# Performance work log

Measured on AMD Instinct MI355X. Metric: run time of the kernel, lower is better.

The kernel has to match this reference:

```python
import jax, jax.numpy as jnp
import numpy as np

D_MODEL = 1024
NUM_HEADS = 16
HEAD_DIM = D_MODEL // NUM_HEADS
B, S = 4, 2048


def setup_inputs() -> dict:
    key = jax.random.key(0)
    ks = jax.random.split(key, 11)
    sc = 1.0 / np.sqrt(D_MODEL)
    return {
        "query": jax.random.normal(ks[0], (B, S, D_MODEL), jnp.float32),
        "key": jax.random.normal(ks[1], (B, S, D_MODEL), jnp.float32),
        "value": jax.random.normal(ks[2], (B, S, D_MODEL), jnp.float32),
        "Wq": jax.random.normal(ks[3], (D_MODEL, D_MODEL), jnp.float32) * sc,
        "bq": jnp.zeros((D_MODEL,), jnp.float32),
        "Wk": jax.random.normal(ks[4], (D_MODEL, D_MODEL), jnp.float32) * sc,
        "bk": jnp.zeros((D_MODEL,), jnp.float32),
        "Wv": jax.random.normal(ks[5], (D_MODEL, D_MODEL), jnp.float32) * sc,
        "bv": jnp.zeros((D_MODEL,), jnp.float32),
        "Wo": jax.random.normal(ks[6], (D_MODEL, D_MODEL), jnp.float32) * sc,
        "bo": jnp.zeros((D_MODEL,), jnp.float32),
    }


def _split_heads(x):
    b, s, _ = x.shape
    return x.reshape(b, s, NUM_HEADS, HEAD_DIM).transpose(0, 2, 1, 3)  # [B,H,S,Dh]


def reference(query, key, value, Wq, bq, Wk, bk, Wv, bv, Wo, bo):
    q = _split_heads(query @ Wq + bq)
    k = _split_heads(key @ Wk + bk)
    v = _split_heads(value @ Wv + bv)
    scores = jnp.einsum("bhqd,bhkd->bhqk", q, k) / np.sqrt(HEAD_DIM)
    attn = jax.nn.softmax(scores, axis=-1)
    out = jnp.einsum("bhqk,bhkd->bhqd", attn, v)
    out = out.transpose(0, 2, 1, 3).reshape(query.shape[0], -1, D_MODEL)
    return out @ Wo + bo
```

## Files before the change

kernel.cpp:

```cpp
#include <hip/hip_runtime.h>

typedef unsigned short u16;
typedef unsigned int   u32;
typedef unsigned long long u64;
typedef __attribute__((ext_vector_type(8))) short bf16x8;
typedef __attribute__((ext_vector_type(4))) float f32x4;

#define S_  2048
#define DH  64
#define DM  1024
#define BS  8192
#define CS  0.18033688011112042f

static __device__ __forceinline__ float bf2f(u16 v){ return __uint_as_float(((u32)v)<<16); }
static __device__ __forceinline__ u16 f2bf(float f){
  u32 x = __float_as_uint(f);
  return (u16)((x + 0x7fffu + ((x>>16)&1u)) >> 16);
}
#if __has_builtin(__builtin_amdgcn_cvt_pk_bf16_f32)
static __device__ __forceinline__ u32 pk2(float x, float y){
  typedef __attribute__((ext_vector_type(2))) __bf16 bf2v;
  union { bf2v v; u32 u; } c; c.v = __builtin_amdgcn_cvt_pk_bf16_f32(x, y); return c.u;
}
#else
static __device__ __forceinline__ u32 pk2(float x, float y){
  return (u32)f2bf(x) | ((u32)f2bf(y) << 16);
}
#endif
#if __has_builtin(__builtin_amdgcn_exp2f)
#define EXP2F(x) __builtin_amdgcn_exp2f(x)
#else
#define EXP2F(x) exp2f(x)
#endif

static __device__ __forceinline__ void dma16(const u16* g, const u16* l){
  __builtin_amdgcn_global_load_lds(
      (const __attribute__((address_space(1))) u32*)(u64)(uintptr_t)g,
      (__attribute__((address_space(3))) u32*)(u32)(u64)(uintptr_t)l, 16, 0, 0);
}

static __device__ __forceinline__ bf16x8 lds_frag(const u16* p){
  union { bf16x8 f; uint2 u[2]; } w;
  w.u[0] = *(const uint2*)(p);
  w.u[1] = *(const uint2*)(p+4);
  return w.f;
}
static __device__ __forceinline__ bf16x8 frag16v(const u16* p){
  union { bf16x8 f; uint4 u; } w;
  w.u = *(const uint4*)p;
  return w.f;
}
static __device__ __forceinline__ void stage16_bf(const u16* __restrict__ g, u16* s){
  uint4 a = *(const uint4*)g;
  uint4 b = *(const uint4*)(g+8);
  *(uint2*)(s+0)  = make_uint2(a.x,a.y);
  *(uint2*)(s+4)  = make_uint2(a.z,a.w);
  *(uint2*)(s+8)  = make_uint2(b.x,b.y);
  *(uint2*)(s+12) = make_uint2(b.z,b.w);
}
static __device__ __forceinline__ void stage16_f32(const float* __restrict__ g, u16* s){
  float4 a0 = ((const float4*)g)[0];
  float4 a1 = ((const float4*)g)[1];
  float4 a2 = ((const float4*)g)[2];
  float4 a3 = ((const float4*)g)[3];
  *(uint2*)(s+0)  = make_uint2(pk2(a0.x,a0.y), pk2(a0.z,a0.w));
  *(uint2*)(s+4)  = make_uint2(pk2(a1.x,a1.y), pk2(a1.z,a1.w));
  *(uint2*)(s+8)  = make_uint2(pk2(a2.x,a2.y), pk2(a2.z,a2.w));
  *(uint2*)(s+12) = make_uint2(pk2(a3.x,a3.y), pk2(a3.z,a3.w));
}

union AFU { bf16x8 f; u32 u[4]; };

__global__ __launch_bounds__(256) void transpose4(const void* __restrict__ i0,
    const void* __restrict__ i1, const void* __restrict__ i2, const void* __restrict__ i3,
    u16* o0, u16* o1, u16* o2, u16* o3, const int f32f){
  __shared__ u16 tile[32][33];
  int z = blockIdx.z;
  const void* in = z==0?i0 : z==1?i1 : z==2?i2 : i3;
  u16* out = z==0?o0 : z==1?o1 : z==2?o2 : o3;
  bool f32 = f32f != 0;
  int tx = threadIdx.x, ty = threadIdx.y;
  int c  = blockIdx.x*32 + tx;
  int r0 = blockIdx.y*32;
  for (int i=ty;i<32;i+=8){
    long off = (long)(r0+i)*DM + c;
    tile[i][tx] = f32 ? f2bf(((const float*)in)[off]) : ((const u16*)in)[off];
  }
  __syncthreads();
  int rr = r0 + tx, c0 = blockIdx.x*32;
  for (int i=ty;i<32;i+=8) out[(long)(c0+i)*DM + rr] = tile[tx][i];
}

__global__ __launch_bounds__(256) void gemm_qkv(
    const void* __restrict__ A0, const void* __restrict__ A1, const void* __restrict__ A2,
    const u16* __restrict__ W0, const u16* __restrict__ W1, const u16* __restrict__ W2,
    const void* __restrict__ bv0, const void* __restrict__ bv1, const void* __restrict__ bv2,
    u16* C0, u16* C1, u16* C2, const int f32f){
  constexpr int AST = 36;
  __shared__ __align__(16) u16 As[128*AST];
  __shared__ __align__(16) u16 Bs[128*32];
  int z = blockIdx.z;
  const void* A  = z==0?A0 : z==1?A1 : A2;
  const u16* BT  = z==0?W0 : z==1?W1 : W2;
  const void* bias = z==0?bv0 : z==1?bv1 : bv2;
  u16* C = z==0?C0 : z==1?C1 : C2;
  const bool aF32 = (f32f != 0);
  int tid = threadIdx.x;
  int by = blockIdx.x, bx = blockIdx.y;
  int lane = tid & 63, w = tid >> 6;
  int t = lane & 15, q = lane >> 4;
  int wr = w >> 1, wc = w & 1;
  f32x4 acc[4][4];
  #pragma unroll
  for(int i=0;i<4;i++) for(int j=0;j<4;j++) for(int k=0;k<4;k++) acc[i][j][k]=0.f;

  const u16* gB = BT + ((long)(bx*128 + w*32 + (lane>>2))*DM + (lane&3)*8);
  const u16* lB = &Bs[(w*32)*32];
  long aoff = (long)(by*128 + (tid>>1))*DM + (tid&1)*16;
  const u16* ArdB = &As[(wr*64 + t)*AST + q*8];
  const u16* BrdB = &Bs[(wc*64 + t)*32  + q*8];

  for (int k0=0; k0<DM; k0+=32){
    dma16(gB + k0, lB);
    dma16(gB + 16*DM + k0, lB + 16*32);
    u16* AsW = &As[(tid>>1)*36 + (tid&1)*16];
    if (aF32) stage16_f32((const float*)A + aoff + k0, AsW);
    else      stage16_bf ((const u16*)A  + aoff + k0, AsW);
    __syncthreads();
    bf16x8 af[4], bfr[4];
    #pragma unroll
    for (int rt=0;rt<4;rt++) af[rt]  = lds_frag(ArdB + rt*16*AST);
    #pragma unroll
    for (int ct=0;ct<4;ct++) bfr[ct] = lds_frag(BrdB + ct*16*32);
    #pragma unroll
    for (int rt=0;rt<4;rt++)
      #pragma unroll
      for (int ct=0;ct<4;ct++)
        acc[rt][ct] = __builtin_amdgcn_mfma_f32_16x16x32_bf16(af[rt], bfr[ct], acc[rt][ct], 0,0,0);
    __syncthreads();
  }
  float scale = (z==0) ? CS : 1.0f;
  #pragma unroll
  for (int ct=0;ct<4;ct++){
    int col = bx*128 + wc*64 + ct*16 + t;
    float bvv = aF32 ? ((const float*)bias)[col] : bf2f(((const u16*)bias)[col]);
    #pragma unroll
    for (int rt=0;rt<4;rt++){
      int row0 = by*128 + wr*64 + rt*16 + q*4;
      if (z == 2){
        int bb = row0 >> 11, s = row0 & 2047;
        long vbase = (long)bb*2097152 + (long)col*2048
                   + (s & ~63) + ((rt>>1)<<5) + (q<<3) + ((rt&1)<<2);
        u32 lo = pk2(acc[rt][ct][0]+bvv, acc[rt][ct][1]+bvv);
        u32 hi = pk2(acc[rt][ct][2]+bvv, acc[rt][ct][3]+bvv);
        *(uint2*)(C + vbase) = make_uint2(lo,hi);
      } else {
        #pragma unroll
        for (int r=0;r<4;r++)
          C[(long)(row0+r)*DM + col] = f2bf((acc[rt][ct][r] + bvv)*scale);
      }
    }
  }
}

__global__ __launch_bounds__(256) void gemm_o(const u16* __restrict__ A,
    const u16* __restrict__ BT, const void* __restrict__ bias, void* __restrict__ C,
    const int f32f){
  __shared__ __align__(16) u16 As[128*32];
  __shared__ __align__(16) u16 Bs[128*32];
  const int f = f32f;
  int tid = threadIdx.x;
  int by = blockIdx.x, bx = blockIdx.y;
  int lane = tid & 63, w = tid >> 6;
  int t = lane & 15, q = lane >> 4;
  int wr = w >> 1, wc = w & 1;
  f32x4 acc[4][4];
  #pragma unroll
  for(int i=0;i<4;i++) for(int j=0;j<4;j++) for(int k=0;k<4;k++) acc[i][j][k]=0.f;

  const u16* gA = A  + ((long)(by*128 + w*32 + (lane>>2))*DM + (lane&3)*8);
  const u16* gB = BT + ((long)(bx*128 + w*32 + (lane>>2))*DM + (lane&3)*8);
  const u16* lA = &As[(w*32)*32];
  const u16* lB = &Bs[(w*32)*32];
  const u16* ArdB = &As[(wr*64 + t)*32 + q*8];
  const u16* BrdB = &Bs[(wc*64 + t)*32 + q*8];

  for (int k0=0; k0<DM; k0+=32){
    dma16(gA + k0, lA);
    dma16(gA + 16*DM + k0, lA + 16*32);
    dma16(gB + k0, lB);
    dma16(gB + 16*DM + k0, lB + 16*32);
    __syncthreads();
    bf16x8 af[4], bfr[4];
    #pragma unroll
    for (int rt=0;rt<4;rt++) af[rt]  = lds_frag(ArdB + rt*16*32);
    #pragma unroll
    for (int ct=0;ct<4;ct++) bfr[ct] = lds_frag(BrdB + ct*16*32);
    #pragma unroll
    for (int rt=0;rt<4;rt++)
      #pragma unroll
      for (int ct=0;ct<4;ct++)
        acc[rt][ct] = __builtin_amdgcn_mfma_f32_16x16x32_bf16(af[rt], bfr[ct], acc[rt][ct], 0,0,0);
    __syncthreads();
  }
  #pragma unroll
  for (int ct=0;ct<4;ct++){
    int col = bx*128 + wc*64 + ct*16 + t;
    float bvv = f ? ((const float*)bias)[col] : bf2f(((const u16*)bias)[col]);
    #pragma unroll
    for (int rt=0;rt<4;rt++){
      int row0 = by*128 + wr*64 + rt*16 + q*4;
      #pragma unroll
      for (int r=0;r<4;r++){
        long idx = (long)(row0+r)*DM + col;
        float v = acc[rt][ct][r] + bvv;
        if (f) ((float*)C)[idx] = v;
        else   ((u16*)C)[idx]  = f2bf(v);
      }
    }
  }
}

static __device__ __forceinline__ void qk16(const u16* Kc, int t, int q, int xorv,
    const bf16x8 (&qf)[2][2], f32x4 (&sacc)[2][4]){
  #pragma unroll
  for (int i=0;i<2;i++)
    #pragma unroll
    for (int j=0;j<4;j++)
      #pragma unroll
      for (int k=0;k<4;k++) sacc[i][j][k]=0.f;
  #pragma unroll
  for (int ks=0; ks<2; ks++){
    int off = ((ks*64 + q*16) ^ xorv) >> 1;
    bf16x8 k0 = frag16v(Kc + (t     )*64 + off);
    bf16x8 k1 = frag16v(Kc + (16 + t)*64 + off);
    bf16x8 k2 = frag16v(Kc + (32 + t)*64 + off);
    bf16x8 k3 = frag16v(Kc + (48 + t)*64 + off);
    __builtin_amdgcn_s_setprio(1);
    #pragma unroll
    for (int rt=0; rt<2; rt++){
      sacc[rt][0] = __builtin_amdgcn_mfma_f32_16x16x32_bf16(k0, qf[rt][ks], sacc[rt][0],0,0,0);
      sacc[rt][1] = __builtin_amdgcn_mfma_f32_16x16x32_bf16(k1, qf[rt][ks], sacc[rt][1],0,0,0);
      sacc[rt][2] = __builtin_amdgcn_mfma_f32_16x16x32_bf16(k2, qf[rt][ks], sacc[rt][2],0,0,0);
      sacc[rt][3] = __builtin_amdgcn_mfma_f32_16x16x32_bf16(k3, qf[rt][ks], sacc[rt][3],0,0,0);
    }
    __builtin_amdgcn_s_setprio(0);
  }
}

static __device__ __forceinline__ void sm16(const f32x4 (&sacc)[2][4], AFU (&af)[2][2]){
  #pragma unroll
  for (int rt=0; rt<2; rt++){
    float ev[4][4];
    #pragma unroll
    for (int c=0; c<4; c++)
      #pragma unroll
      for (int r=0; r<4; r++) ev[c][r] = EXP2F(sacc[rt][c][r]);
    #pragma unroll
    for (int ks=0; ks<2; ks++){
      af[rt][ks].u[0] = pk2(ev[2*ks  ][0], ev[2*ks  ][1]);
      af[rt][ks].u[1] = pk2(ev[2*ks  ][2], ev[2*ks  ][3]);
      af[rt][ks].u[2] = pk2(ev[2*ks+1][0], ev[2*ks+1][1]);
      af[rt][ks].u[3] = pk2(ev[2*ks+1][2], ev[2*ks+1][3]);
    }
  }
}

static __device__ __forceinline__ void pv16(const u16* Vc, int t, int q, int xorv,
    const AFU (&af)[2][2], bf16x8 vonef, f32x4 (&o)[2][4], f32x4 (&o4)[2]){
  #pragma unroll
  for (int ks=0; ks<2; ks++){
    int off = ((ks*64 + q*16) ^ xorv) >> 1;
    bf16x8 v0 = frag16v(Vc + (t     )*64 + off);
    bf16x8 v1 = frag16v(Vc + (16 + t)*64 + off);
    bf16x8 v2 = frag16v(Vc + (32 + t)*64 + off);
    bf16x8 v3 = frag16v(Vc + (48 + t)*64 + off);
    __builtin_amdgcn_s_setprio(1);
    #pragma unroll
    for (int rt=0; rt<2; rt++){
      o[rt][0] = __builtin_amdgcn_mfma_f32_16x16x32_bf16(af[rt][ks].f, v0, o[rt][0],0,0,0);
      o[rt][1] = __builtin_amdgcn_mfma_f32_16x16x32_bf16(af[rt][ks].f, v1, o[rt][1],0,0,0);
      o[rt][2] = __builtin_amdgcn_mfma_f32_16x16x32_bf16(af[rt][ks].f, v2, o[rt][2],0,0,0);
      o[rt][3] = __builtin_amdgcn_mfma_f32_16x16x32_bf16(af[rt][ks].f, v3, o[rt][3],0,0,0);
      o4[rt]   = __builtin_amdgcn_mfma_f32_16x16x32_bf16(af[rt][ks].f, vonef, o4[rt],0,0,0);
    }
    __builtin_amdgcn_s_setprio(0);
  }
}

__global__ __launch_bounds__(256,4) void attn6(const u16* __restrict__ Q,
    const u16* __restrict__ Kb, const u16* __restrict__ Vt, u16* __restrict__ O){
  __shared__ __align__(16) u16 SM_[20480];
  const int VB = 12288;
  int tid = threadIdx.x;
  int bid = blockIdx.x;
  int qt = bid >> 6;
  int s6 = bid & 63;
  int bh = (s6 & 7)*8 + (s6 >> 3);
  int b = bh >> 4, h = bh & 15;
  int lane = tid & 63, w = tid >> 6;
  int t = lane & 15, q = lane >> 4;

  const u16* Qbase = Q + ((long)(b*S_ + qt*128 + w*32 + t)*DM + h*DH + q*8);
  bf16x8 qf[2][2];
  qf[0][0] = frag16v(Qbase);
  qf[0][1] = frag16v(Qbase + 32);
  qf[1][0] = frag16v(Qbase + 16*DM);
  qf[1][1] = frag16v(Qbase + 16*DM + 32);

  int r0 = tid >> 3;
  int cb = ((tid & 7) * 16) ^ ((r0 & 7) << 4);
  const char* gK = (const char*)Kb + (((long)(b*S_ + r0)*DM + h*DH) << 1) + cb;
  const char* gV = (const char*)Vt + ((((long)bh << 17) + ((long)r0 << 11)) << 1) + cb;
  const long gK1 = ((long)32*DM) << 1;
  const long gV1 = ((long)32*S_) << 1;
  const long KT  = ((long)64*DM) << 1;
  const int ld0 = w*512, ld1 = 2048 + w*512;

  f32x4 o[2][4];
  #pragma unroll
  for (int i=0;i<2;i++)
    #pragma unroll
    for (int j=0;j<4;j++)
      #pragma unroll
      for (int k=0;k<4;k++) o[i][j][k]=0.f;
  f32x4 o4[2];
  #pragma unroll
  for (int i=0;i<2;i++)
    #pragma unroll
    for (int k=0;k<4;k++) o4[i][k]=0.f;

  union { bf16x8 f; u32 u[4]; } vone;
  { u32 ovv = (t==0) ? 0x3F803F80u : 0u;
    vone.u[0]=ovv; vone.u[1]=ovv; vone.u[2]=ovv; vone.u[3]=ovv; }

  const int xorv = (t & 7) << 4;

  dma16((const u16*)(gK),            &SM_[ld0]);
  dma16((const u16*)(gK + gK1),      &SM_[ld1]);
  dma16((const u16*)(gV),            &SM_[VB + ld0]);
  dma16((const u16*)(gV + gV1),      &SM_[VB + ld1]);
  dma16((const u16*)(gK + KT),       &SM_[4096 + ld0]);
  dma16((const u16*)(gK + KT + gK1), &SM_[4096 + ld1]);
  asm volatile("s_waitcnt vmcnt(4)" ::: "memory");
  __builtin_amdgcn_s_barrier();

  f32x4 sacc[2][4];
  AFU af[2][2];
  qk16(&SM_[0], t, q, xorv, qf, sacc);
  sm16(sacc, af);
  dma16((const u16*)(gK + 2*KT),       &SM_[8192 + ld0]);
  dma16((const u16*)(gK + 2*KT + gK1), &SM_[8192 + ld1]);
  dma16((const u16*)(gV + (1L<<7)),        &SM_[VB + 4096 + ld0]);
  dma16((const u16*)(gV + (1L<<7) + gV1),  &SM_[VB + 4096 + ld1]);

  int kcur = 4096, knx = 8192, kfree = 0;
  for (int kt = 1; kt < 32; kt++){
    asm volatile("s_waitcnt vmcnt(4)" ::: "memory");
    __builtin_amdgcn_s_barrier();
    if (kt <= 30){
      int nk = (kt+2 < 32) ? (kt+2) : 31;
      const char* g = gK + (long)nk*KT;
      dma16((const u16*)(g),       &SM_[kfree + ld0]);
      dma16((const u16*)(g + gK1), &SM_[kfree + ld1]);
    }
    qk16(&SM_[kcur], t, q, xorv, qf, sacc);
    pv16(&SM_[VB + (((kt-1)&1)<<12)], t, q, xorv, af, vone.f, o, o4);
    sm16(sacc, af);
    __builtin_amdgcn_s_barrier();
    if (kt <= 30){
      const char* g = gV + ((long)(kt+1) << 7);
      dma16((const u16*)(g),       &SM_[VB + (((kt+1)&1)<<12) + ld0]);
      dma16((const u16*)(g + gV1), &SM_[VB + (((kt+1)&1)<<12) + ld1]);
    }
    int tmp = kcur; kcur = knx; knx = kfree; kfree = tmp;
  }
  asm volatile("s_waitcnt vmcnt(0)" ::: "memory");
  __builtin_amdgcn_s_barrier();
  pv16(&SM_[VB + 4096], t, q, xorv, af, vone.f, o, o4);

  #pragma unroll
  for (int rt=0; rt<2; rt++){
    #pragma unroll
    for (int r=0; r<4; r++){
      float l = __shfl(o4[rt][r], lane & 48);
      float inv = 1.f / l;
      int row = qt*128 + w*32 + rt*16 + q*4 + r;
      #pragma unroll
      for (int ct=0; ct<4; ct++)
        O[(long)(b*S_ + row)*DM + h*DH + ct*16 + t] = f2bf(o[rt][ct][r] * inv);
    }
  }
}

extern "C" void kernel_launch(void* const* d_in, const int* in_sizes, int n_in,
                              void* d_out, int out_size, void* d_ws, size_t ws_size,
                              hipStream_t stream){
  (void)n_in; (void)out_size; (void)ws_size;
  const void* xq = d_in[0];
  const void* xk = d_in[1];
  const void* xv = d_in[2];
  const void* Wq = d_in[3];
  const void* bq = d_in[4];
  const void* Wk = d_in[5];
  const void* bk = d_in[6];
  const void* Wv = d_in[7];
  const void* bv = d_in[8];
  const void* Wo = d_in[9];
  const void* bo = d_in[10];

  const long NT = (long)BS*DM;
  int f32f = 1;
  if (in_sizes && in_sizes[0] == (int)(NT*2)) f32f = 0;

  u16* base = (u16*)((char*)d_ws + 256);
  u16* Qb  = base;
  u16* Kbf = base + NT;
  u16* Vt  = base + 2*NT;
  u16* WqT = base + 3*NT;
  u16* WkT = WqT + (long)DM*DM;
  u16* WvT = WkT + (long)DM*DM;
  u16* WoT = WvT + (long)DM*DM;

  dim3 gb(256,1,1);
  transpose4<<<dim3(32,32,4), dim3(32,8,1), 0, stream>>>(Wq, Wk, Wv, Wo,
      WqT, WkT, WvT, WoT, f32f);

  gemm_qkv<<<dim3(64,8,3), gb, 0, stream>>>(xq, xk, xv,
      WqT, WkT, WvT, bq, bk, bv, Qb, Kbf, Vt, f32f);

  attn6<<<dim3(1024,1,1), gb, 0, stream>>>(Qb, Kbf, Vt, Qb );

  gemm_o<<<dim3(64,8,1), gb, 0, stream>>>(Qb, WoT, bo, d_out, f32f);
}
```

Before: 403.7 us.

## Pre-convert activations to bf16 and double-buffer DMA in projection GEMMs

The weight-transpose kernel becomes a prep kernel that also converts the fp32 query/key/value activations to bf16 in workspace. When the workspace is large enough, the QKV GEMM can then load A through the same async DMA path as B. Both QKV and output GEMMs now double-buffer LDS and prefetch the next K-slice while computing the current one, using waitcnt and raw barriers. This adds an extra full pass over the activations and needs more workspace, in exchange for overlapping global loads with MFMA work.

```diff
diff --git a/kernel.cpp b/kernel.cpp
--- a/kernel.cpp
+++ b/kernel.cpp
@@ -71,40 +71,63 @@
 
 union AFU { bf16x8 f; u32 u[4]; };
 
-__global__ __launch_bounds__(256) void transpose4(const void* __restrict__ i0,
-    const void* __restrict__ i1, const void* __restrict__ i2, const void* __restrict__ i3,
-    u16* o0, u16* o1, u16* o2, u16* o3, const int f32f){
+__global__ __launch_bounds__(256) void prep(
+    const void* __restrict__ w0, const void* __restrict__ w1,
+    const void* __restrict__ w2, const void* __restrict__ w3,
+    u16* t0, u16* t1, u16* t2, u16* t3,
+    const void* __restrict__ a0, const void* __restrict__ a1,
+    const void* __restrict__ a2,
+    u16* c0, u16* c1, u16* c2, const int f32f){
   __shared__ u16 tile[32][33];
   int z = blockIdx.z;
-  const void* in = z==0?i0 : z==1?i1 : z==2?i2 : i3;
-  u16* out = z==0?o0 : z==1?o1 : z==2?o2 : o3;
+  int tid = threadIdx.x;
   bool f32 = f32f != 0;
-  int tx = threadIdx.x, ty = threadIdx.y;
-  int c  = blockIdx.x*32 + tx;
-  int r0 = blockIdx.y*32;
-  for (int i=ty;i<32;i+=8){
-    long off = (long)(r0+i)*DM + c;
-    tile[i][tx] = f32 ? f2bf(((const float*)in)[off]) : ((const u16*)in)[off];
-  }
-  __syncthreads();
-  int rr = r0 + tx, c0 = blockIdx.x*32;
-  for (int i=ty;i<32;i+=8) out[(long)(c0+i)*DM + rr] = tile[tx][i];
-}
-
+  if (z < 4){
+    const void* in = z==0?w0 : z==1?w1 : z==2?w2 : w3;
+    u16* out = z==0?t0 : z==1?t1 : z==2?t2 : t3;
+    int tx = tid & 31, ty = tid >> 5;
+    int c  = blockIdx.x*32 + tx;
+    int r0 = blockIdx.y*32;
+    for (int i=ty;i<32;i+=8){
+      long off = (long)(r0+i)*DM + c;
+      tile[i][tx] = f32 ? f2bf(((const float*)in)[off]) : ((const u16*)in)[off];
+    }
+    __syncthreads();
+    int rr = r0 + tx, cb = blockIdx.x*32;
+    for (int i=ty;i<32;i+=8) out[(long)(cb+i)*DM + rr] = tile[tx][i];
+  } else {
+    if (!f32) return;
+    const void* in = z==4?a0 : z==5?a1 : a2;
+    u16* out = z==4?c0 : z==5?c1 : c2;
+    long lb = (long)blockIdx.y*32 + blockIdx.x;
+    long base = (lb*256 + tid)*8;
+    #pragma unroll
+    for (int it=0; it<4; it++){
+      long i = base + (long)it*2097152;
+      const float4* p = (const float4*)((const float*)in + i);
+      float4 x = p[0], y = p[1];
+      *(uint4*)(out + i) = make_uint4(pk2(x.x,x.y), pk2(x.z,x.w), pk2(y.x,y.y), pk2(y.z,y.w));
+    }
+  }
+}
+
+template<int ADMA>
 __global__ __launch_bounds__(256) void gemm_qkv(
     const void* __restrict__ A0, const void* __restrict__ A1, const void* __restrict__ A2,
     const u16* __restrict__ W0, const u16* __restrict__ W1, const u16* __restrict__ W2,
     const void* __restrict__ bv0, const void* __restrict__ bv1, const void* __restrict__ bv2,
     u16* C0, u16* C1, u16* C2, const int f32f){
-  constexpr int AST = 36;
-  __shared__ __align__(16) u16 As[128*AST];
-  __shared__ __align__(16) u16 Bs[128*32];
+  constexpr int AST = ADMA ? 32 : 36;
+  constexpr int NB  = ADMA ? 2 : 1;
+  __shared__ __align__(16) u16 As[NB][128*AST];
+  __shared__ __align__(16) u16 Bs[NB][128*32];
   int z = blockIdx.z;
   const void* A  = z==0?A0 : z==1?A1 : A2;
   const u16* BT  = z==0?W0 : z==1?W1 : W2;
   const void* bias = z==0?bv0 : z==1?bv1 : bv2;
   u16* C = z==0?C0 : z==1?C1 : C2;
-  const bool aF32 = (f32f != 0);
+  const bool aF32 = (!ADMA) && (f32f != 0);
+  const bool bF32 = (f32f != 0);
   int tid = threadIdx.x;
   int by = blockIdx.x, bx = blockIdx.y;
   int lane = tid & 63, w = tid >> 6;
@@ -115,35 +138,70 @@
   for(int i=0;i<4;i++) for(int j=0;j<4;j++) for(int k=0;k<4;k++) acc[i][j][k]=0.f;
 
   const u16* gB = BT + ((long)(bx*128 + w*32 + (lane>>2))*DM + (lane&3)*8);
-  const u16* lB = &Bs[(w*32)*32];
-  long aoff = (long)(by*128 + (tid>>1))*DM + (tid&1)*16;
-  const u16* ArdB = &As[(wr*64 + t)*AST + q*8];
-  const u16* BrdB = &Bs[(wc*64 + t)*32  + q*8];
-
-  for (int k0=0; k0<DM; k0+=32){
-    dma16(gB + k0, lB);
-    dma16(gB + 16*DM + k0, lB + 16*32);
-    u16* AsW = &As[(tid>>1)*36 + (tid&1)*16];
-    if (aF32) stage16_f32((const float*)A + aoff + k0, AsW);
-    else      stage16_bf ((const u16*)A  + aoff + k0, AsW);
-    __syncthreads();
-    bf16x8 af[4], bfr[4];
-    #pragma unroll
-    for (int rt=0;rt<4;rt++) af[rt]  = lds_frag(ArdB + rt*16*AST);
-    #pragma unroll
-    for (int ct=0;ct<4;ct++) bfr[ct] = lds_frag(BrdB + ct*16*32);
-    #pragma unroll
-    for (int rt=0;rt<4;rt++)
-      #pragma unroll
-      for (int ct=0;ct<4;ct++)
-        acc[rt][ct] = __builtin_amdgcn_mfma_f32_16x16x32_bf16(af[rt], bfr[ct], acc[rt][ct], 0,0,0);
-    __syncthreads();
-  }
+
+  if constexpr (ADMA){
+    const u16* gA = (const u16*)A + ((long)(by*128 + w*32 + (lane>>2))*DM + (lane&3)*8);
+    const int lb = (w*32)*32;
+    dma16(gA,         &As[0][lb]);
+    dma16(gA + 16*DM, &As[0][lb + 16*32]);
+    dma16(gB,         &Bs[0][lb]);
+    dma16(gB + 16*DM, &Bs[0][lb + 16*32]);
+    for (int k0=0; k0<DM; k0+=32){
+      int cur = (k0>>5)&1;
+      if (k0+32 < DM){
+        dma16(gA + k0+32,         &As[cur^1][lb]);
+        dma16(gA + k0+32 + 16*DM, &As[cur^1][lb + 16*32]);
+        dma16(gB + k0+32,         &Bs[cur^1][lb]);
+        dma16(gB + k0+32 + 16*DM, &Bs[cur^1][lb + 16*32]);
+        asm volatile("s_waitcnt vmcnt(4)" ::: "memory");
+      } else {
+        asm volatile("s_waitcnt vmcnt(0)" ::: "memory");
+      }
+      __builtin_amdgcn_s_barrier();
+      bf16x8 af[4], bfr[4];
+      const u16* Ar = &As[cur][(wr*64 + t)*32 + q*8];
+      const u16* Br = &Bs[cur][(wc*64 + t)*32 + q*8];
+      #pragma unroll
+      for (int rt=0;rt<4;rt++) af[rt]  = frag16v(Ar + rt*16*32);
+      #pragma unroll
+      for (int ct=0;ct<4;ct++) bfr[ct] = frag16v(Br + ct*16*32);
+      #pragma unroll
+      for (int rt=0;rt<4;rt++)
+        #pragma unroll
+        for (int ct=0;ct<4;ct++)
+          acc[rt][ct] = __builtin_amdgcn_mfma_f32_16x16x32_bf16(af[rt], bfr[ct], acc[rt][ct], 0,0,0);
+      __builtin_amdgcn_s_barrier();
+    }
+  } else {
+    long aoff = (long)(by*128 + (tid>>1))*DM + (tid&1)*16;
+    const u16* ArdB = &As[0][(wr*64 + t)*AST + q*8];
+    const u16* BrdB = &Bs[0][(wc*64 + t)*32  + q*8];
+    for (int k0=0; k0<DM; k0+=32){
+      dma16(gB + k0,         &Bs[0][(w*32)*32]);
+      dma16(gB + 16*DM + k0, &Bs[0][(w*32)*32 + 16*32]);
+      u16* AsW = &As[0][(tid>>1)*36 + (tid&1)*16];
+      if (aF32) stage16_f32((const float*)A + aoff + k0, AsW);
+      else      stage16_bf ((const u16*)A  + aoff + k0, AsW);
+      __syncthreads();
+      bf16x8 af[4], bfr[4];
+      #pragma unroll
+      for (int rt=0;rt<4;rt++) af[rt]  = lds_frag(ArdB + rt*16*AST);
+      #pragma unroll
+      for (int ct=0;ct<4;ct++) bfr[ct] = lds_frag(BrdB + ct*16*32);
+      #pragma unroll
+      for (int rt=0;rt<4;rt++)
+        #pragma unroll
+        for (int ct=0;ct<4;ct++)
+          acc[rt][ct] = __builtin_amdgcn_mfma_f32_16x16x32_bf16(af[rt], bfr[ct], acc[rt][ct], 0,0,0);
+      __syncthreads();
+    }
+  }
+
   float scale = (z==0) ? CS : 1.0f;
   #pragma unroll
   for (int ct=0;ct<4;ct++){
     int col = bx*128 + wc*64 + ct*16 + t;
-    float bvv = aF32 ? ((const float*)bias)[col] : bf2f(((const u16*)bias)[col]);
+    float bvv = bF32 ? ((const float*)bias)[col] : bf2f(((const u16*)bias)[col]);
     #pragma unroll
     for (int rt=0;rt<4;rt++){
       int row0 = by*128 + wr*64 + rt*16 + q*4;
@@ -166,8 +224,8 @@
 __global__ __launch_bounds__(256) void gemm_o(const u16* __restrict__ A,
     const u16* __restrict__ BT, const void* __restrict__ bias, void* __restrict__ C,
     const int f32f){
-  __shared__ __align__(16) u16 As[128*32];
-  __shared__ __align__(16) u16 Bs[128*32];
+  __shared__ __align__(16) u16 As[2][128*32];
+  __shared__ __align__(16) u16 Bs[2][128*32];
   const int f = f32f;
   int tid = threadIdx.x;
   int by = blockIdx.x, bx = blockIdx.y;
@@ -180,28 +238,36 @@
 
   const u16* gA = A  + ((long)(by*128 + w*32 + (lane>>2))*DM + (lane&3)*8);
   const u16* gB = BT + ((long)(bx*128 + w*32 + (lane>>2))*DM + (lane&3)*8);
-  const u16* lA = &As[(w*32)*32];
-  const u16* lB = &Bs[(w*32)*32];
-  const u16* ArdB = &As[(wr*64 + t)*32 + q*8];
-  const u16* BrdB = &Bs[(wc*64 + t)*32 + q*8];
-
+  const int lb = (w*32)*32;
+  dma16(gA,         &As[0][lb]);
+  dma16(gA + 16*DM, &As[0][lb + 16*32]);
+  dma16(gB,         &Bs[0][lb]);
+  dma16(gB + 16*DM, &Bs[0][lb + 16*32]);
   for (int k0=0; k0<DM; k0+=32){
-    dma16(gA + k0, lA);
-    dma16(gA + 16*DM + k0, lA + 16*32);
-    dma16(gB + k0, lB);
-    dma16(gB + 16*DM + k0, lB + 16*32);
-    __syncthreads();
+    int cur = (k0>>5)&1;
+    if (k0+32 < DM){
+      dma16(gA + k0+32,         &As[cur^1][lb]);
+      dma16(gA + k0+32 + 16*DM, &As[cur^1][lb + 16*32]);
+      dma16(gB + k0+32,         &Bs[cur^1][lb]);
+      dma16(gB + k0+32 + 16*DM, &Bs[cur^1][lb + 16*32]);
+      asm volatile("s_waitcnt vmcnt(4)" ::: "memory");
+    } else {
+      asm volatile("s_waitcnt vmcnt(0)" ::: "memory");
+    }
+    __builtin_amdgcn_s_barrier();
     bf16x8 af[4], bfr[4];
-    #pragma unroll
-    for (int rt=0;rt<4;rt++) af[rt]  = lds_frag(ArdB + rt*16*32);
-    #pragma unroll
-    for (int ct=0;ct<4;ct++) bfr[ct] = lds_frag(BrdB + ct*16*32);
+    const u16* Ar = &As[cur][(wr*64 + t)*32 + q*8];
+    const u16* Br = &Bs[cur][(wc*64 + t)*32 + q*8];
+    #pragma unroll
+    for (int rt=0;rt<4;rt++) af[rt]  = frag16v(Ar + rt*16*32);
+    #pragma unroll
+    for (int ct=0;ct<4;ct++) bfr[ct] = frag16v(Br + ct*16*32);
     #pragma unroll
     for (int rt=0;rt<4;rt++)
       #pragma unroll
       for (int ct=0;ct<4;ct++)
         acc[rt][ct] = __builtin_amdgcn_mfma_f32_16x16x32_bf16(af[rt], bfr[ct], acc[rt][ct], 0,0,0);
-    __syncthreads();
+    __builtin_amdgcn_s_barrier();
   }
   #pragma unroll
   for (int ct=0;ct<4;ct++){
@@ -396,7 +462,7 @@
 extern "C" void kernel_launch(void* const* d_in, const int* in_sizes, int n_in,
                               void* d_out, int out_size, void* d_ws, size_t ws_size,
                               hipStream_t stream){
-  (void)n_in; (void)out_size; (void)ws_size;
+  (void)n_in; (void)out_size;
   const void* xq = d_in[0];
   const void* xk = d_in[1];
   const void* xv = d_in[2];
@@ -421,13 +487,27 @@
   u16* WkT = WqT + (long)DM*DM;
   u16* WvT = WkT + (long)DM*DM;
   u16* WoT = WvT + (long)DM*DM;
+  u16* Xc0 = WoT + (long)DM*DM;
+  u16* Xc1 = Xc0 + NT;
+  u16* Xc2 = Xc1 + NT;
+  size_t need_pre = 256 + (size_t)(6*NT + 4*(long)DM*DM)*2;
+  bool pre = ws_size >= need_pre;
 
   dim3 gb(256,1,1);
-  transpose4<<<dim3(32,32,4), dim3(32,8,1), 0, stream>>>(Wq, Wk, Wv, Wo,
-      WqT, WkT, WvT, WoT, f32f);
-
-  gemm_qkv<<<dim3(64,8,3), gb, 0, stream>>>(xq, xk, xv,
-      WqT, WkT, WvT, bq, bk, bv, Qb, Kbf, Vt, f32f);
+  int nz = (pre && f32f) ? 7 : 4;
+  prep<<<dim3(32,32,nz), gb, 0, stream>>>(Wq, Wk, Wv, Wo,
+      WqT, WkT, WvT, WoT, xq, xk, xv, Xc0, Xc1, Xc2, f32f);
+
+  if (pre){
+    const void* Aq = f32f ? (const void*)Xc0 : xq;
+    const void* Ak = f32f ? (const void*)Xc1 : xk;
+    const void* Av = f32f ? (const void*)Xc2 : xv;
+    gemm_qkv<1><<<dim3(64,8,3), gb, 0, stream>>>(Aq, Ak, Av,
+        WqT, WkT, WvT, bq, bk, bv, Qb, Kbf, Vt, f32f);
+  } else {
+    gemm_qkv<0><<<dim3(64,8,3), gb, 0, stream>>>(xq, xk, xv,
+        WqT, WkT, WvT, bq, bk, bv, Qb, Kbf, Vt, f32f);
+  }
 
   attn6<<<dim3(1024,1,1), gb, 0, stream>>>(Qb, Kbf, Vt, Qb );
 
```

New measurement: 375.1 us. -7.1%, faster.
